# Performance work log

Measured on AMD Instinct MI355X. Metric: run time of the kernel, lower is better.

## Reference

```python
import jax, jax.numpy as jnp
import numpy as np

B, C, N, H, S = 2048, 64, 64, 8, 4
D = C // H          # head dim 8
CS = C // S         # per-scale channels 16
CP = C // 4         # pattern memory dim 16


def _conv1d(x, w, b):
    # x: [B, Cin, N], w: [Cout, Cin, 3], 'same' padding
    y = jax.lax.conv_general_dilated(x, w, (1,), ((1, 1),),
                                     dimension_numbers=('NCH', 'OIH', 'NCH'))
    return y + b[None, :, None]


def setup_inputs() -> dict:
    key = jax.random.key(0)
    ks = jax.random.split(key, 20)
    s = 0.05
    f32 = jnp.float32
    return {
        'x': jax.random.normal(ks[0], (B, C, N), f32),
        'points': jax.random.normal(ks[1], (N, 3), f32),
        'conv1_w': jax.random.normal(ks[2], (S, CS, C, 3), f32) * s,
        'conv1_b': jnp.zeros((S, CS), f32),
        'conv2_w': jax.random.normal(ks[3], (S, CS, CS, 3), f32) * s,
        'conv2_b': jnp.zeros((S, CS), f32),
        'pattern_memory': jax.random.normal(ks[4], (64, CP), f32),
        'pm1_w': jax.random.normal(ks[5], (C, C + CP), f32) * s,
        'pm1_b': jnp.zeros((C,), f32),
        'pm2_w': jax.random.normal(ks[6], (C, C), f32) * s,
        'pm2_b': jnp.zeros((C,), f32),
        'q_w': jax.random.normal(ks[7], (C, C), f32) * s,
        'q_b': jnp.zeros((C,), f32),
        'k_w': jax.random.normal(ks[8], (C, C), f32) * s,
        'k_b': jnp.zeros((C,), f32),
        'v_w': jax.random.normal(ks[9], (C, C), f32) * s,
        'v_b': jnp.zeros((C,), f32),
        'in_w': jax.random.normal(ks[10], (3 * C, C), f32) * s,
        'in_b': jnp.zeros((3 * C,), f32),
        'mo_w': jax.random.normal(ks[11], (C, C), f32) * s,
        'mo_b': jnp.zeros((C,), f32),
        'out_w': jax.random.normal(ks[12], (C, C), f32) * s,
        'out_b': jnp.zeros((C,), f32),
        'ln_g': jnp.ones((C,), f32),
        'ln_beta': jnp.zeros((C,), f32),
        'adjacency': jax.random.randint(ks[13], (64, 64), 0, 2, jnp.int32),
    }


def _forward(x, points, conv1_w, conv1_b, conv2_w, conv2_b, pattern_memory,
             pm1_w, pm1_b, pm2_w, pm2_b, q_w, q_b, k_w, k_b, v_w, v_b,
             in_w, in_b, mo_w, mo_b, out_w, out_b, ln_g, ln_beta, adjacency):
    b, c, n = x.shape
    # multi-scale conv stacks (fixed small loop over scales)
    feats = []
    for i in range(S):
        y = jax.nn.relu(_conv1d(x, conv1_w[i], conv1_b[i]))
        y = jax.nn.relu(_conv1d(y, conv2_w[i], conv2_b[i]))
        feats.append(jnp.transpose(y, (0, 2, 1)))  # [B, N, CS]
    combined = jnp.concatenate(feats, axis=-1)     # [B, N, C]
    # pattern memory broadcast per point (N == 64)
    pat = jnp.broadcast_to(pattern_memory[None], (b, n, CP))
    pi = jnp.concatenate([combined, pat], axis=-1)  # [B, N, C+CP]
    pf = jax.nn.relu(pi @ pm1_w.T + pm1_b) @ pm2_w.T + pm2_b  # [B, N, C]
    q = pf @ q_w.T + q_b
    k = pf @ k_w.T + k_b
    v = pf @ v_w.T + v_b
    # nn.MultiheadAttention: internal in_proj + out_proj
    wq, wk, wv = in_w[:C], in_w[C:2 * C], in_w[2 * C:]
    bq, bk, bv = in_b[:C], in_b[C:2 * C], in_b[2 * C:]
    q2 = (q @ wq.T + bq).reshape(b, n, H, D)
    k2 = (k @ wk.T + bk).reshape(b, n, H, D)
    v2 = (v @ wv.T + bv).reshape(b, n, H, D)
    scale = 1.0 / np.sqrt(D).astype(np.float32)
    scores = jnp.einsum('bnhd,bmhd->bhnm', q2, k2) * scale
    attn = jax.nn.softmax(scores, axis=-1)
    ctx = jnp.einsum('bhnm,bmhd->bnhd', attn, v2).reshape(b, n, C)
    attended = ctx @ mo_w.T + mo_b
    # vectorized geometric bias (replaces the 64x64 python loop)
    diff = points[:, None, :] - points[None, :, :]
    dist = jnp.sqrt(jnp.sum(diff * diff, axis=-1) + 1e-12)
    geo = jnp.where(adjacency > 0, jnp.float32(0.5), -0.1 / (1.0 + dist))
    attended = attended + geo[None]
    # layer norm over channels, then output projection
    h = attended + pf
    mu = jnp.mean(h, axis=-1, keepdims=True)
    var = jnp.mean((h - mu) ** 2, axis=-1, keepdims=True)
    hn = (h - mu) * jax.lax.rsqrt(var + 1e-5) * ln_g + ln_beta
    out = hn @ out_w.T + out_b
    return jnp.transpose(out, (0, 2, 1))  # [B, C, N]


def reference(x, points, conv1_w, conv1_b, conv2_w, conv2_b, pattern_memory,
              pm1_w, pm1_b, pm2_w, pm2_b, q_w, q_b, k_w, k_b, v_w, v_b,
              in_w, in_b, mo_w, mo_b, out_w, out_b, ln_g, ln_beta, adjacency):
    return _forward(x, points, conv1_w, conv1_b, conv2_w, conv2_b,
                    pattern_memory, pm1_w, pm1_b, pm2_w, pm2_b, q_w, q_b,
                    k_w, k_b, v_w, v_b, in_w, in_b, mo_w, mo_b, out_w, out_b,
                    ln_g, ln_beta, adjacency)
```

## Files before the change

### kernel.cpp

```cpp
#include <hip/hip_runtime.h>
#include <math.h>

using bf16x8 = __attribute__((ext_vector_type(8))) __bf16;
using f32x4  = __attribute__((ext_vector_type(4))) float;

#if __has_builtin(__builtin_amdgcn_exp2f)
#define EXP2F(x) __builtin_amdgcn_exp2f(x)
#else
#define EXP2F(x) exp2f(x)
#endif

__device__ __forceinline__ unsigned short f2bf(float f) {
  unsigned u = __float_as_uint(f);
  unsigned r = u + 0x7fffu + ((u >> 16) & 1u);
  return (unsigned short)(r >> 16);
}

__device__ __forceinline__ unsigned cvt_pk_bf16(float a, float b) {
  unsigned r;
  asm("v_cvt_pk_bf16_f32 %0, %1, %2" : "=v"(r) : "v"(a), "v"(b));
  return r;
}
__device__ __forceinline__ uint2 pk4(float a, float b, float c, float d) {
  uint2 r; r.x = cvt_pk_bf16(a, b); r.y = cvt_pk_bf16(c, d); return r;
}

__device__ __forceinline__ f32x4 mfma16(uint4 a, uint4 b, f32x4 c) {
  return __builtin_amdgcn_mfma_f32_16x16x32_bf16(
      __builtin_bit_cast(bf16x8, a), __builtin_bit_cast(bf16x8, b), c, 0, 0, 0);
}
__device__ __forceinline__ float swz_xor16(float v) {
  return __int_as_float(__builtin_amdgcn_ds_swizzle(__float_as_int(v), 0x401F));
}

#define FRAG_OFF(k, n) (((((n) >> 4) * 2 + ((k) >> 5)) * 64 + (((k) >> 3) & 3) * 16 + ((n) & 15)) * 8 + ((k) & 7))

#define ATT_C 0.51006997f

__global__ void precompute_kernel(
    const float* __restrict__ conv1_w, const float* __restrict__ conv2_w,
    const float* __restrict__ pm1_w, const float* __restrict__ pm1_b,
    const float* __restrict__ pm2_w,
    const float* __restrict__ q_w, const float* __restrict__ q_b,
    const float* __restrict__ k_w, const float* __restrict__ k_b,
    const float* __restrict__ v_w, const float* __restrict__ v_b,
    const float* __restrict__ in_w, const float* __restrict__ in_b,
    const float* __restrict__ mo_w, const float* __restrict__ out_w,
    const float* __restrict__ pattern, const float* __restrict__ points,
    const int* __restrict__ adjacency,
    unsigned short* __restrict__ wsb, float* __restrict__ wsf) {
  int idx = blockIdx.x * 256 + threadIdx.x;
  if (idx < 12288) {
    int t = idx >> 12, rem = idx & 4095;
    int oc = rem >> 6, c = rem & 63;
    wsb[idx] = f2bf(conv1_w[(oc * 64 + c) * 3 + t]);
  } else if (idx < 24576) {
    int i2 = idx - 12288;
    int t = i2 >> 12, rem = i2 & 4095;
    int oc = rem >> 6, ci = rem & 63;
    float v = ((ci >> 4) == (oc >> 4)) ? conv2_w[(oc * 16 + (ci & 15)) * 3 + t] : 0.0f;
    wsb[idx] = f2bf(v);
  } else if (idx < 28672) {
    int rem = idx - 24576;
    wsb[idx] = f2bf(pm1_w[(rem >> 6) * 80 + (rem & 63)]);
  } else if (idx < 32768) {
    wsb[idx] = f2bf(pm2_w[idx - 28672]);
  } else if (idx < 36864) {
    int rem = idx - 32768; int c = rem >> 6, k = rem & 63;
    float s = 0.f;
    #pragma unroll 8
    for (int j = 0; j < 64; ++j) s += in_w[c * 64 + j] * q_w[j * 64 + k];
    wsb[idx] = f2bf(s * ATT_C);
  } else if (idx < 40960) {
    int rem = idx - 36864; int c = rem >> 6, k = rem & 63;
    float s = 0.f;
    #pragma unroll 8
    for (int j = 0; j < 64; ++j) s += in_w[(64 + c) * 64 + j] * k_w[j * 64 + k];
    wsb[idx] = f2bf(s);
  } else if (idx < 45056) {
    int rem = idx - 40960; int c = rem >> 6, k = rem & 63;
    float s = 0.f;
    #pragma unroll 8
    for (int j = 0; j < 64; ++j) s += in_w[(128 + c) * 64 + j] * v_w[j * 64 + k];
    wsb[idx] = f2bf(s);
  } else if (idx < 49152) {
    wsb[idx] = f2bf(mo_w[idx - 45056]);
  } else if (idx < 53248) {
    wsb[idx] = f2bf(out_w[idx - 49152]);
  } else if (idx < 57344) {
    int rem = idx - 53248; int c = rem >> 6, n = rem & 63;
    float s = pm1_b[c];
    #pragma unroll
    for (int cp = 0; cp < 16; ++cp) s += pm1_w[c * 80 + 64 + cp] * pattern[n * 16 + cp];
    wsf[rem] = s;
  } else if (idx < 61440) {
    int rem = idx - 57344; int c = rem >> 6, n = rem & 63;
    float dd = 1e-12f;
    #pragma unroll
    for (int i = 0; i < 3; ++i) { float d = points[n * 3 + i] - points[c * 3 + i]; dd += d * d; }
    float dist = sqrtf(dd);
    wsf[4096 + rem] = (adjacency[n * 64 + c] > 0) ? 0.5f : (-0.1f / (1.0f + dist));
  } else if (idx < 61632) {
    int rem = idx - 61440; int which = rem >> 6, c = rem & 63;
    if (which == 0) {
      float s = in_b[c];
      for (int j = 0; j < 64; ++j) s += in_w[c * 64 + j] * q_b[j];
      wsf[8192 + c] = s * ATT_C;
    } else if (which == 1) {
      float s = in_b[64 + c];
      for (int j = 0; j < 64; ++j) s += in_w[(64 + c) * 64 + j] * k_b[j];
      wsf[8256 + c] = s;
    } else {
      float s = in_b[128 + c];
      for (int j = 0; j < 64; ++j) s += in_w[(128 + c) * 64 + j] * v_b[j];
      wsf[8320 + c] = s;
    }
  }
}

__device__ __forceinline__ void gemm64(const unsigned short* __restrict__ Wg,
                                       const unsigned short* Bf,
                                       int w, int lane, f32x4 acc[4]) {
  const int l15 = lane & 15, lq = lane >> 4;
  #pragma unroll
  for (int s = 0; s < 2; ++s) {
    bf16x8 a = *reinterpret_cast<const bf16x8*>(Wg + (16 * w + l15) * 64 + s * 32 + lq * 8);
    #pragma unroll
    for (int nt = 0; nt < 4; ++nt) {
      bf16x8 bb = *reinterpret_cast<const bf16x8*>(Bf + ((nt * 2 + s) * 64 + lane) * 8);
      acc[nt] = __builtin_amdgcn_mfma_f32_16x16x32_bf16(a, bb, acc[nt], 0, 0, 0);
    }
  }
}

#define SLOT_B 4096
#define KBASE  8704
#define VBASE  13312
#define H32F   2048
#define LNS    6656

__global__ __launch_bounds__(256, 4) void fused_kernel(
    const float* __restrict__ x,
    const unsigned short* __restrict__ wsb, const float* __restrict__ wsf,
    const float* __restrict__ conv1_b, const float* __restrict__ conv2_b,
    const float* __restrict__ pm2_b, const float* __restrict__ mo_b,
    const float* __restrict__ out_b, const float* __restrict__ ln_g,
    const float* __restrict__ ln_beta, float* __restrict__ out) {
  __shared__ __align__(16) unsigned char smem_raw[35840];
  unsigned short* S16 = reinterpret_cast<unsigned short*>(smem_raw);
  float* S32 = reinterpret_cast<float*>(smem_raw);

  const int tid = threadIdx.x;
  const int b = blockIdx.x;
  const int lane = tid & 63;
  const int w = tid >> 6;
  const int l15 = lane & 15;
  const int lq = lane >> 4;
  const int c0 = 16 * w + lq * 4;
  f32x4 pfs[4];

  if (tid < 8) S16[VBASE + tid] = 0;
  {
    const float* xb = x + b * 4096 + w * 16 * 64 + lane;
    float v[16];
    #pragma unroll
    for (int j = 0; j < 16; ++j) v[j] = xb[j * 64];
    #pragma unroll
    for (int g = 0; g < 2; ++g) {
      uint4 u;
      u.x = cvt_pk_bf16(v[g * 8 + 0], v[g * 8 + 1]);
      u.y = cvt_pk_bf16(v[g * 8 + 2], v[g * 8 + 3]);
      u.z = cvt_pk_bf16(v[g * 8 + 4], v[g * 8 + 5]);
      u.w = cvt_pk_bf16(v[g * 8 + 6], v[g * 8 + 7]);
      *reinterpret_cast<uint4*>(S16 + FRAG_OFF(w * 16 + g * 8, lane)) = u;
    }
  }
  __syncthreads();

  auto conv_pass = [&](const unsigned short* Wg, int srcBase, f32x4 acc[4]) {
    bf16x8 a6[3][2];
    #pragma unroll
    for (int t = 0; t < 3; ++t)
      #pragma unroll
      for (int s = 0; s < 2; ++s)
        a6[t][s] = *reinterpret_cast<const bf16x8*>(Wg + t * 4096 + (16 * w + l15) * 64 + s * 32 + lq * 8);
    #pragma unroll
    for (int nt = 0; nt < 4; ++nt) {
      #pragma unroll
      for (int t = 0; t < 3; ++t) {
        int np = nt * 16 + l15 + (t - 1);
        bool ok = (unsigned)np < 64u;
        int a = srcBase + (((np >> 4) * 2) * 64 + lq * 16 + (np & 15)) * 8;
        int A0 = ok ? a : VBASE;
        int A1 = ok ? (a + 512) : VBASE;
        bf16x8 b0 = *reinterpret_cast<const bf16x8*>(S16 + A0);
        bf16x8 b1 = *reinterpret_cast<const bf16x8*>(S16 + A1);
        acc[nt] = __builtin_amdgcn_mfma_f32_16x16x32_bf16(a6[t][0], b0, acc[nt], 0, 0, 0);
        acc[nt] = __builtin_amdgcn_mfma_f32_16x16x32_bf16(a6[t][1], b1, acc[nt], 0, 0, 0);
      }
    }
  };

  {
    f32x4 acc[4] = {};
    conv_pass(wsb, 0, acc);
    float bia[4] = {conv1_b[c0], conv1_b[c0 + 1], conv1_b[c0 + 2], conv1_b[c0 + 3]};
    #pragma unroll
    for (int nt = 0; nt < 4; ++nt) {
      int n = nt * 16 + l15;
      uint2 u = pk4(fmaxf(acc[nt][0] + bia[0], 0.f), fmaxf(acc[nt][1] + bia[1], 0.f),
                    fmaxf(acc[nt][2] + bia[2], 0.f), fmaxf(acc[nt][3] + bia[3], 0.f));
      *reinterpret_cast<uint2*>(S16 + SLOT_B + FRAG_OFF(c0, n)) = u;
    }
  }
  __syncthreads();

  {
    f32x4 acc[4] = {};
    conv_pass(wsb + 12288, SLOT_B, acc);
    float bia[4] = {conv2_b[c0], conv2_b[c0 + 1], conv2_b[c0 + 2], conv2_b[c0 + 3]};
    #pragma unroll
    for (int nt = 0; nt < 4; ++nt) {
      int n = nt * 16 + l15;
      uint2 u = pk4(fmaxf(acc[nt][0] + bia[0], 0.f), fmaxf(acc[nt][1] + bia[1], 0.f),
                    fmaxf(acc[nt][2] + bia[2], 0.f), fmaxf(acc[nt][3] + bia[3], 0.f));
      *reinterpret_cast<uint2*>(S16 + FRAG_OFF(c0, n)) = u;
    }
  }
  __syncthreads();

  {
    f32x4 acc[4] = {};
    gemm64(wsb + 24576, S16, w, lane, acc);
    #pragma unroll
    for (int nt = 0; nt < 4; ++nt) {
      int n = nt * 16 + l15;
      uint2 u = pk4(fmaxf(acc[nt][0] + wsf[(c0 + 0) * 64 + n], 0.f),
                    fmaxf(acc[nt][1] + wsf[(c0 + 1) * 64 + n], 0.f),
                    fmaxf(acc[nt][2] + wsf[(c0 + 2) * 64 + n], 0.f),
                    fmaxf(acc[nt][3] + wsf[(c0 + 3) * 64 + n], 0.f));
      *reinterpret_cast<uint2*>(S16 + SLOT_B + FRAG_OFF(c0, n)) = u;
    }
  }
  __syncthreads();

  {
    f32x4 acc[4] = {};
    gemm64(wsb + 28672, S16 + SLOT_B, w, lane, acc);
    float bia[4] = {pm2_b[c0], pm2_b[c0 + 1], pm2_b[c0 + 2], pm2_b[c0 + 3]};
    #pragma unroll
    for (int nt = 0; nt < 4; ++nt) {
      int n = nt * 16 + l15;
      f32x4 v;
      #pragma unroll
      for (int r = 0; r < 4; ++r) v[r] = acc[nt][r] + bia[r];
      pfs[nt] = v;
      *reinterpret_cast<uint2*>(S16 + FRAG_OFF(c0, n)) = pk4(v[0], v[1], v[2], v[3]);
    }
  }
  __syncthreads();

  {
    f32x4 acc[4] = {};
    gemm64(wsb + 32768, S16, w, lane, acc);
    #pragma unroll
    for (int nt = 0; nt < 4; ++nt) {
      int n = nt * 16 + l15;
      *reinterpret_cast<uint2*>(S16 + SLOT_B + n * 72 + c0) =
          pk4(acc[nt][0] + wsf[8192 + c0], acc[nt][1] + wsf[8192 + c0 + 1],
              acc[nt][2] + wsf[8192 + c0 + 2], acc[nt][3] + wsf[8192 + c0 + 3]);
    }
  }
  {
    f32x4 acc[4] = {};
    gemm64(wsb + 36864, S16, w, lane, acc);
    #pragma unroll
    for (int nt = 0; nt < 4; ++nt) {
      int n = nt * 16 + l15;
      *reinterpret_cast<uint2*>(S16 + KBASE + n * 72 + c0) =
          pk4(acc[nt][0] + wsf[8256 + c0], acc[nt][1] + wsf[8256 + c0 + 1],
              acc[nt][2] + wsf[8256 + c0 + 2], acc[nt][3] + wsf[8256 + c0 + 3]);
    }
  }
  {
    f32x4 acc[4] = {};
    gemm64(wsb + 40960, S16, w, lane, acc);
    #pragma unroll
    for (int nt = 0; nt < 4; ++nt) {
      int n = nt * 16 + l15;
      #pragma unroll
      for (int r = 0; r < 4; ++r)
        S16[VBASE + (c0 + r) * 72 + n] = f2bf(acc[nt][r] + wsf[8320 + c0 + r]);
    }
  }
  __syncthreads();

  {
    uint4 vb[2][2];
    #pragma unroll
    for (int rr = 0; rr < 2; ++rr) {
      int h = w + rr * 4;
      #pragma unroll
      for (int ks = 0; ks < 2; ++ks)
        vb[rr][ks] = *reinterpret_cast<const uint4*>(
            S16 + VBASE + (h * 8 + (l15 & 7)) * 72 + ks * 32 + lq * 8);
    }
    __syncthreads();

    const int Pb = VBASE + w * 1152;
    const bool lq0 = (lq == 0);
    #pragma unroll
    for (int rr = 0; rr < 2; ++rr) {
      const int h = w + rr * 4;
      uint4 ka[4];
      #pragma unroll
      for (int mt = 0; mt < 4; ++mt) {
        uint4 t = *reinterpret_cast<const uint4*>(S16 + KBASE + (mt * 16 + l15) * 72 + h * 8);
        ka[mt].x = lq0 ? t.x : 0u; ka[mt].y = lq0 ? t.y : 0u;
        ka[mt].z = lq0 ? t.z : 0u; ka[mt].w = lq0 ? t.w : 0u;
      }
      #pragma unroll
      for (int q = 0; q < 4; ++q) {
        uint4 qb = *reinterpret_cast<const uint4*>(S16 + SLOT_B + (q * 16 + l15) * 72 + h * 8);
        qb.x = lq0 ? qb.x : 0u; qb.y = lq0 ? qb.y : 0u;
        qb.z = lq0 ? qb.z : 0u; qb.w = lq0 ? qb.w : 0u;
        f32x4 sc[4];
        #pragma unroll
        for (int mt = 0; mt < 4; ++mt) {
          f32x4 z = {0.f, 0.f, 0.f, 0.f};
          sc[mt] = mfma16(ka[mt], qb, z);
        }
        float sum = 0.f;
        #pragma unroll
        for (int mt = 0; mt < 4; ++mt)
          #pragma unroll
          for (int r = 0; r < 4; ++r) {
            float e = EXP2F(sc[mt][r]);
            sc[mt][r] = e; sum += e;
          }
        sum += swz_xor16(sum);
        sum += __shfl_xor(sum, 32);
        float inv = __builtin_amdgcn_rcpf(sum);
        #pragma unroll
        for (int mt = 0; mt < 4; ++mt) {
          unsigned d0 = __builtin_amdgcn_perm(__float_as_uint(sc[mt][1] * inv),
                                              __float_as_uint(sc[mt][0] * inv), 0x07060302u);
          unsigned d1 = __builtin_amdgcn_perm(__float_as_uint(sc[mt][3] * inv),
                                              __float_as_uint(sc[mt][2] * inv), 0x07060302u);
          *reinterpret_cast<uint2*>(S16 + Pb + l15 * 72 + mt * 16 + lq * 4) = make_uint2(d0, d1);
        }
        f32x4 ctx = {0.f, 0.f, 0.f, 0.f};
        #pragma unroll
        for (int ks = 0; ks < 2; ++ks) {
          uint4 pa = *reinterpret_cast<const uint4*>(S16 + Pb + l15 * 72 + ks * 32 + lq * 8);
          ctx = mfma16(pa, vb[rr][ks], ctx);
        }
        if (l15 < 8) {
          const int kk = h * 8 + l15;
          #pragma unroll
          for (int r = 0; r < 4; ++r)
            S16[FRAG_OFF(kk, q * 16 + lq * 4 + r)] = f2bf(ctx[r]);
        }
      }
    }
  }
  __syncthreads();

  {
    f32x4 acc[4] = {};
    gemm64(wsb + 45056, S16, w, lane, acc);
    #pragma unroll
    for (int nt = 0; nt < 4; ++nt) {
      int n = nt * 16 + l15;
      #pragma unroll
      for (int r = 0; r < 4; ++r) {
        int c = c0 + r;
        S32[H32F + c * 65 + n] = acc[nt][r] + mo_b[c] + wsf[4096 + c * 64 + n] + pfs[nt][r];
      }
    }
  }
  __syncthreads();

  {
    int n = tid & 63, qq = tid >> 6;
    float sum = 0.f, ssq = 0.f;
    #pragma unroll
    for (int j = 0; j < 16; ++j) {
      float v = S32[H32F + (qq * 16 + j) * 65 + n];
      sum += v; ssq += v * v;
    }
    S32[LNS + tid] = sum;
    S32[LNS + 256 + tid] = ssq;
    __syncthreads();
    if (tid < 64) {
      float s = S32[LNS + tid] + S32[LNS + 64 + tid] + S32[LNS + 128 + tid] + S32[LNS + 192 + tid];
      float ss = S32[LNS + 256 + tid] + S32[LNS + 320 + tid] + S32[LNS + 384 + tid] + S32[LNS + 448 + tid];
      float mu = s * (1.0f / 64.0f);
      float var = ss * (1.0f / 64.0f) - mu * mu;
      S32[LNS + 512 + tid] = mu;
      S32[LNS + 576 + tid] = rsqrtf(var + 1e-5f);
    }
    __syncthreads();
    float mu = S32[LNS + 512 + n], rs = S32[LNS + 576 + n];
    #pragma unroll
    for (int half = 0; half < 2; ++half) {
      int ch0 = qq * 16 + half * 8;
      float vv[8];
      #pragma unroll
      for (int jj = 0; jj < 8; ++jj) {
        int c = ch0 + jj;
        vv[jj] = (S32[H32F + c * 65 + n] - mu) * rs * ln_g[c] + ln_beta[c];
      }
      uint4 u;
      u.x = cvt_pk_bf16(vv[0], vv[1]);
      u.y = cvt_pk_bf16(vv[2], vv[3]);
      u.z = cvt_pk_bf16(vv[4], vv[5]);
      u.w = cvt_pk_bf16(vv[6], vv[7]);
      *reinterpret_cast<uint4*>(S16 + FRAG_OFF(ch0, n)) = u;
    }
  }
  __syncthreads();

  {
    f32x4 acc[4] = {};
    gemm64(wsb + 49152, S16, w, lane, acc);
    float* ob = out + b * 4096;
    float bia[4] = {out_b[c0], out_b[c0 + 1], out_b[c0 + 2], out_b[c0 + 3]};
    #pragma unroll
    for (int nt = 0; nt < 4; ++nt) {
      int n = nt * 16 + l15;
      #pragma unroll
      for (int r = 0; r < 4; ++r)
        ob[(c0 + r) * 64 + n] = acc[nt][r] + bia[r];
    }
  }
}

extern "C" void kernel_launch(void* const* d_in, const int* in_sizes, int n_in,
                              void* d_out, int out_size, void* d_ws, size_t ws_size,
                              hipStream_t stream) {
  const float* x        = (const float*)d_in[0];
  const float* points   = (const float*)d_in[1];
  const float* conv1_w  = (const float*)d_in[2];
  const float* conv1_b  = (const float*)d_in[3];
  const float* conv2_w  = (const float*)d_in[4];
  const float* conv2_b  = (const float*)d_in[5];
  const float* pattern  = (const float*)d_in[6];
  const float* pm1_w    = (const float*)d_in[7];
  const float* pm1_b    = (const float*)d_in[8];
  const float* pm2_w    = (const float*)d_in[9];
  const float* pm2_b    = (const float*)d_in[10];
  const float* q_w      = (const float*)d_in[11];
  const float* q_b      = (const float*)d_in[12];
  const float* k_w      = (const float*)d_in[13];
  const float* k_b      = (const float*)d_in[14];
  const float* v_w      = (const float*)d_in[15];
  const float* v_b      = (const float*)d_in[16];
  const float* in_w     = (const float*)d_in[17];
  const float* in_b     = (const float*)d_in[18];
  const float* mo_w     = (const float*)d_in[19];
  const float* mo_b     = (const float*)d_in[20];
  const float* out_w    = (const float*)d_in[21];
  const float* out_b    = (const float*)d_in[22];
  const float* ln_g     = (const float*)d_in[23];
  const float* ln_beta  = (const float*)d_in[24];
  const int*   adjacency= (const int*)d_in[25];

  unsigned short* wsb = (unsigned short*)d_ws;
  float* wsf = (float*)((char*)d_ws + 106496);

  precompute_kernel<<<241, 256, 0, stream>>>(
      conv1_w, conv2_w, pm1_w, pm1_b, pm2_w, q_w, q_b, k_w, k_b, v_w, v_b,
      in_w, in_b, mo_w, out_w, pattern, points, adjacency, wsb, wsf);

  fused_kernel<<<2048, 256, 0, stream>>>(
      x, wsb, wsf, conv1_b, conv2_b, pm2_b, mo_b, out_b, ln_g, ln_beta,
      (float*)d_out);
}
```

Measured before the change: 169.1 us.

## Replace padded LDS rows with XOR swizzle to fit five blocks per CU

Q/K/V/P tiles in shared memory drop the 72-element padded stride for a dense 64-element stride with an XOR swizzle on the column offset, and the fp32 layernorm buffer loses its 65-stride padding. LDS shrinks from 35840 to 32768 bytes and the launch bound rises from 4 to 5 blocks per CU to raise occupancy. The V projection is recomputed transposed (activations as A operand, weights as B) so it can be written with packed vector stores instead of scalar bf16 stores. The unpadded fp32 buffer and a tighter register budget risk more bank conflicts or spills.

```diff
diff --git a/kernel.cpp b/kernel.cpp
--- a/kernel.cpp
+++ b/kernel.cpp
@@ -134,19 +134,19 @@
 }
 
 #define SLOT_B 4096
-#define KBASE  8704
-#define VBASE  13312
+#define KBASE  8192
+#define VBASE  12288
 #define H32F   2048
-#define LNS    6656
-
-__global__ __launch_bounds__(256, 4) void fused_kernel(
+#define LNS    6144
+
+__global__ __launch_bounds__(256, 5) void fused_kernel(
     const float* __restrict__ x,
     const unsigned short* __restrict__ wsb, const float* __restrict__ wsf,
     const float* __restrict__ conv1_b, const float* __restrict__ conv2_b,
     const float* __restrict__ pm2_b, const float* __restrict__ mo_b,
     const float* __restrict__ out_b, const float* __restrict__ ln_g,
     const float* __restrict__ ln_beta, float* __restrict__ out) {
-  __shared__ __align__(16) unsigned char smem_raw[35840];
+  __shared__ __align__(16) unsigned char smem_raw[32768];
   unsigned short* S16 = reinterpret_cast<unsigned short*>(smem_raw);
   float* S32 = reinterpret_cast<float*>(smem_raw);
 
@@ -157,6 +157,7 @@
   const int l15 = lane & 15;
   const int lq = lane >> 4;
   const int c0 = 16 * w + lq * 4;
+  const int xorm = (l15 & 7) << 3;
   f32x4 pfs[4];
 
   if (tid < 8) S16[VBASE + tid] = 0;
@@ -266,7 +267,7 @@
     #pragma unroll
     for (int nt = 0; nt < 4; ++nt) {
       int n = nt * 16 + l15;
-      *reinterpret_cast<uint2*>(S16 + SLOT_B + n * 72 + c0) =
+      *reinterpret_cast<uint2*>(S16 + SLOT_B + n * 64 + (c0 ^ xorm)) =
           pk4(acc[nt][0] + wsf[8192 + c0], acc[nt][1] + wsf[8192 + c0 + 1],
               acc[nt][2] + wsf[8192 + c0 + 2], acc[nt][3] + wsf[8192 + c0 + 3]);
     }
@@ -277,20 +278,30 @@
     #pragma unroll
     for (int nt = 0; nt < 4; ++nt) {
       int n = nt * 16 + l15;
-      *reinterpret_cast<uint2*>(S16 + KBASE + n * 72 + c0) =
+      *reinterpret_cast<uint2*>(S16 + KBASE + n * 64 + (c0 ^ xorm)) =
           pk4(acc[nt][0] + wsf[8256 + c0], acc[nt][1] + wsf[8256 + c0 + 1],
               acc[nt][2] + wsf[8256 + c0 + 2], acc[nt][3] + wsf[8256 + c0 + 3]);
     }
   }
   {
     f32x4 acc[4] = {};
-    gemm64(wsb + 40960, S16, w, lane, acc);
-    #pragma unroll
-    for (int nt = 0; nt < 4; ++nt) {
-      int n = nt * 16 + l15;
-      #pragma unroll
-      for (int r = 0; r < 4; ++r)
-        S16[VBASE + (c0 + r) * 72 + n] = f2bf(acc[nt][r] + wsf[8320 + c0 + r]);
+    const unsigned short* AV = wsb + 40960;
+    #pragma unroll
+    for (int s = 0; s < 2; ++s) {
+      bf16x8 a = *reinterpret_cast<const bf16x8*>(S16 + ((w * 2 + s) * 64 + lane) * 8);
+      #pragma unroll
+      for (int ct = 0; ct < 4; ++ct) {
+        bf16x8 bb = *reinterpret_cast<const bf16x8*>(AV + (ct * 16 + l15) * 64 + s * 32 + lq * 8);
+        acc[ct] = __builtin_amdgcn_mfma_f32_16x16x32_bf16(a, bb, acc[ct], 0, 0, 0);
+      }
+    }
+    const int m0 = 16 * w + lq * 4;
+    #pragma unroll
+    for (int ct = 0; ct < 4; ++ct) {
+      int c = ct * 16 + l15;
+      float bia = wsf[8320 + c];
+      *reinterpret_cast<uint2*>(S16 + VBASE + c * 64 + (m0 ^ xorm)) =
+          pk4(acc[ct][0] + bia, acc[ct][1] + bia, acc[ct][2] + bia, acc[ct][3] + bia);
     }
   }
   __syncthreads();
@@ -303,11 +314,11 @@
       #pragma unroll
       for (int ks = 0; ks < 2; ++ks)
         vb[rr][ks] = *reinterpret_cast<const uint4*>(
-            S16 + VBASE + (h * 8 + (l15 & 7)) * 72 + ks * 32 + lq * 8);
+            S16 + VBASE + (h * 8 + (l15 & 7)) * 64 + ((ks * 32 + lq * 8) ^ xorm));
     }
     __syncthreads();
 
-    const int Pb = VBASE + w * 1152;
+    const int Pb = VBASE + w * 1024;
     const bool lq0 = (lq == 0);
     #pragma unroll
     for (int rr = 0; rr < 2; ++rr) {
@@ -315,13 +326,15 @@
       uint4 ka[4];
       #pragma unroll
       for (int mt = 0; mt < 4; ++mt) {
-        uint4 t = *reinterpret_cast<const uint4*>(S16 + KBASE + (mt * 16 + l15) * 72 + h * 8);
+        uint4 t = *reinterpret_cast<const uint4*>(
+            S16 + KBASE + (mt * 16 + l15) * 64 + ((h * 8) ^ xorm));
         ka[mt].x = lq0 ? t.x : 0u; ka[mt].y = lq0 ? t.y : 0u;
         ka[mt].z = lq0 ? t.z : 0u; ka[mt].w = lq0 ? t.w : 0u;
       }
       #pragma unroll
       for (int q = 0; q < 4; ++q) {
-        uint4 qb = *reinterpret_cast<const uint4*>(S16 + SLOT_B + (q * 16 + l15) * 72 + h * 8);
+        uint4 qb = *reinterpret_cast<const uint4*>(
+            S16 + SLOT_B + (q * 16 + l15) * 64 + ((h * 8) ^ xorm));
         qb.x = lq0 ? qb.x : 0u; qb.y = lq0 ? qb.y : 0u;
         qb.z = lq0 ? qb.z : 0u; qb.w = lq0 ? qb.w : 0u;
         f32x4 sc[4];
@@ -347,12 +360,14 @@
                                               __float_as_uint(sc[mt][0] * inv), 0x07060302u);
           unsigned d1 = __builtin_amdgcn_perm(__float_as_uint(sc[mt][3] * inv),
                                               __float_as_uint(sc[mt][2] * inv), 0x07060302u);
-          *reinterpret_cast<uint2*>(S16 + Pb + l15 * 72 + mt * 16 + lq * 4) = make_uint2(d0, d1);
+          *reinterpret_cast<uint2*>(S16 + Pb + l15 * 64 + ((mt * 16 + lq * 4) ^ xorm)) =
+              make_uint2(d0, d1);
         }
         f32x4 ctx = {0.f, 0.f, 0.f, 0.f};
         #pragma unroll
         for (int ks = 0; ks < 2; ++ks) {
-          uint4 pa = *reinterpret_cast<const uint4*>(S16 + Pb + l15 * 72 + ks * 32 + lq * 8);
+          uint4 pa = *reinterpret_cast<const uint4*>(
+              S16 + Pb + l15 * 64 + ((ks * 32 + lq * 8) ^ xorm));
           ctx = mfma16(pa, vb[rr][ks], ctx);
         }
         if (l15 < 8) {
@@ -375,7 +390,7 @@
       #pragma unroll
       for (int r = 0; r < 4; ++r) {
         int c = c0 + r;
-        S32[H32F + c * 65 + n] = acc[nt][r] + mo_b[c] + wsf[4096 + c * 64 + n] + pfs[nt][r];
+        S32[H32F + c * 64 + n] = acc[nt][r] + mo_b[c] + wsf[4096 + c * 64 + n] + pfs[nt][r];
       }
     }
   }
@@ -386,7 +401,7 @@
     float sum = 0.f, ssq = 0.f;
     #pragma unroll
     for (int j = 0; j < 16; ++j) {
-      float v = S32[H32F + (qq * 16 + j) * 65 + n];
+      float v = S32[H32F + (qq * 16 + j) * 64 + n];
       sum += v; ssq += v * v;
     }
     S32[LNS + tid] = sum;
@@ -409,7 +424,7 @@
       #pragma unroll
       for (int jj = 0; jj < 8; ++jj) {
         int c = ch0 + jj;
-        vv[jj] = (S32[H32F + c * 65 + n] - mu) * rs * ln_g[c] + ln_beta[c];
+        vv[jj] = (S32[H32F + c * 64 + n] - mu) * rs * ln_g[c] + ln_beta[c];
       }
       uint4 u;
       u.x = cvt_pk_bf16(vv[0], vv[1]);
```

Result: slower. 183.5 us (+8.5%).

## Split fused kernel across 8 waves with 2D wave tiling and one head per wave

Applied to the files above, without the earlier changes.

Doubles the block to 512 threads and splits each 64x64 GEMM tile between two waves along N, giving each wave two accumulator tiles instead of four. In attention, each wave now handles one head instead of two, and the P scratch buffers are moved onto the K region once K has been loaded into registers. The goal is more resident waves per CU to hide MFMA and LDS latency. The trade-off is extra barrier cost and tight register limits from launch_bounds(512, 8), which could cause spills.

```diff
diff --git a/kernel.cpp b/kernel.cpp
--- a/kernel.cpp
+++ b/kernel.cpp
@@ -120,15 +120,16 @@
 
 __device__ __forceinline__ void gemm64(const unsigned short* __restrict__ Wg,
                                        const unsigned short* Bf,
-                                       int w, int lane, f32x4 acc[4]) {
+                                       int wm, int wn, int lane, f32x4 acc[2]) {
   const int l15 = lane & 15, lq = lane >> 4;
   #pragma unroll
   for (int s = 0; s < 2; ++s) {
-    bf16x8 a = *reinterpret_cast<const bf16x8*>(Wg + (16 * w + l15) * 64 + s * 32 + lq * 8);
-    #pragma unroll
-    for (int nt = 0; nt < 4; ++nt) {
+    bf16x8 a = *reinterpret_cast<const bf16x8*>(Wg + (16 * wm + l15) * 64 + s * 32 + lq * 8);
+    #pragma unroll
+    for (int nti = 0; nti < 2; ++nti) {
+      int nt = 2 * wn + nti;
       bf16x8 bb = *reinterpret_cast<const bf16x8*>(Bf + ((nt * 2 + s) * 64 + lane) * 8);
-      acc[nt] = __builtin_amdgcn_mfma_f32_16x16x32_bf16(a, bb, acc[nt], 0, 0, 0);
+      acc[nti] = __builtin_amdgcn_mfma_f32_16x16x32_bf16(a, bb, acc[nti], 0, 0, 0);
     }
   }
 }
@@ -139,7 +140,7 @@
 #define H32F   2048
 #define LNS    6656
 
-__global__ __launch_bounds__(256, 4) void fused_kernel(
+__global__ __launch_bounds__(512, 8) void fused_kernel(
     const float* __restrict__ x,
     const unsigned short* __restrict__ wsb, const float* __restrict__ wsf,
     const float* __restrict__ conv1_b, const float* __restrict__ conv2_b,
@@ -154,38 +155,38 @@
   const int b = blockIdx.x;
   const int lane = tid & 63;
   const int w = tid >> 6;
+  const int wm = w >> 1;
+  const int wn = w & 1;
   const int l15 = lane & 15;
   const int lq = lane >> 4;
-  const int c0 = 16 * w + lq * 4;
-  f32x4 pfs[4];
+  const int c0 = 16 * wm + lq * 4;
+  f32x4 pfs[2];
 
   if (tid < 8) S16[VBASE + tid] = 0;
   {
-    const float* xb = x + b * 4096 + w * 16 * 64 + lane;
-    float v[16];
-    #pragma unroll
-    for (int j = 0; j < 16; ++j) v[j] = xb[j * 64];
-    #pragma unroll
-    for (int g = 0; g < 2; ++g) {
-      uint4 u;
-      u.x = cvt_pk_bf16(v[g * 8 + 0], v[g * 8 + 1]);
-      u.y = cvt_pk_bf16(v[g * 8 + 2], v[g * 8 + 3]);
-      u.z = cvt_pk_bf16(v[g * 8 + 4], v[g * 8 + 5]);
-      u.w = cvt_pk_bf16(v[g * 8 + 6], v[g * 8 + 7]);
-      *reinterpret_cast<uint4*>(S16 + FRAG_OFF(w * 16 + g * 8, lane)) = u;
-    }
-  }
-  __syncthreads();
-
-  auto conv_pass = [&](const unsigned short* Wg, int srcBase, f32x4 acc[4]) {
+    const float* xb = x + b * 4096 + w * 8 * 64 + lane;
+    float v[8];
+    #pragma unroll
+    for (int j = 0; j < 8; ++j) v[j] = xb[j * 64];
+    uint4 u;
+    u.x = cvt_pk_bf16(v[0], v[1]);
+    u.y = cvt_pk_bf16(v[2], v[3]);
+    u.z = cvt_pk_bf16(v[4], v[5]);
+    u.w = cvt_pk_bf16(v[6], v[7]);
+    *reinterpret_cast<uint4*>(S16 + FRAG_OFF(w * 8, lane)) = u;
+  }
+  __syncthreads();
+
+  auto conv_pass = [&](const unsigned short* Wg, int srcBase, f32x4 acc[2]) {
     bf16x8 a6[3][2];
     #pragma unroll
     for (int t = 0; t < 3; ++t)
       #pragma unroll
       for (int s = 0; s < 2; ++s)
-        a6[t][s] = *reinterpret_cast<const bf16x8*>(Wg + t * 4096 + (16 * w + l15) * 64 + s * 32 + lq * 8);
-    #pragma unroll
-    for (int nt = 0; nt < 4; ++nt) {
+        a6[t][s] = *reinterpret_cast<const bf16x8*>(Wg + t * 4096 + (16 * wm + l15) * 64 + s * 32 + lq * 8);
+    #pragma unroll
+    for (int nti = 0; nti < 2; ++nti) {
+      int nt = 2 * wn + nti;
       #pragma unroll
       for (int t = 0; t < 3; ++t) {
         int np = nt * 16 + l15 + (t - 1);
@@ -195,187 +196,180 @@
         int A1 = ok ? (a + 512) : VBASE;
         bf16x8 b0 = *reinterpret_cast<const bf16x8*>(S16 + A0);
         bf16x8 b1 = *reinterpret_cast<const bf16x8*>(S16 + A1);
-        acc[nt] = __builtin_amdgcn_mfma_f32_16x16x32_bf16(a6[t][0], b0, acc[nt], 0, 0, 0);
-        acc[nt] = __builtin_amdgcn_mfma_f32_16x16x32_bf16(a6[t][1], b1, acc[nt], 0, 0, 0);
+        acc[nti] = __builtin_amdgcn_mfma_f32_16x16x32_bf16(a6[t][0], b0, acc[nti], 0, 0, 0);
+        acc[nti] = __builtin_amdgcn_mfma_f32_16x16x32_bf16(a6[t][1], b1, acc[nti], 0, 0, 0);
       }
     }
   };
 
   {
-    f32x4 acc[4] = {};
+    f32x4 acc[2] = {};
     conv_pass(wsb, 0, acc);
     float bia[4] = {conv1_b[c0], conv1_b[c0 + 1], conv1_b[c0 + 2], conv1_b[c0 + 3]};
     #pragma unroll
-    for (int nt = 0; nt < 4; ++nt) {
-      int n = nt * 16 + l15;
-      uint2 u = pk4(fmaxf(acc[nt][0] + bia[0], 0.f), fmaxf(acc[nt][1] + bia[1], 0.f),
-                    fmaxf(acc[nt][2] + bia[2], 0.f), fmaxf(acc[nt][3] + bia[3], 0.f));
+    for (int nti = 0; nti < 2; ++nti) {
+      int n = (2 * wn + nti) * 16 + l15;
+      uint2 u = pk4(fmaxf(acc[nti][0] + bia[0], 0.f), fmaxf(acc[nti][1] + bia[1], 0.f),
+                    fmaxf(acc[nti][2] + bia[2], 0.f), fmaxf(acc[nti][3] + bia[3], 0.f));
       *reinterpret_cast<uint2*>(S16 + SLOT_B + FRAG_OFF(c0, n)) = u;
     }
   }
   __syncthreads();
 
   {
-    f32x4 acc[4] = {};
+    f32x4 acc[2] = {};
     conv_pass(wsb + 12288, SLOT_B, acc);
     float bia[4] = {conv2_b[c0], conv2_b[c0 + 1], conv2_b[c0 + 2], conv2_b[c0 + 3]};
     #pragma unroll
-    for (int nt = 0; nt < 4; ++nt) {
-      int n = nt * 16 + l15;
-      uint2 u = pk4(fmaxf(acc[nt][0] + bia[0], 0.f), fmaxf(acc[nt][1] + bia[1], 0.f),
-                    fmaxf(acc[nt][2] + bia[2], 0.f), fmaxf(acc[nt][3] + bia[3], 0.f));
+    for (int nti = 0; nti < 2; ++nti) {
+      int n = (2 * wn + nti) * 16 + l15;
+      uint2 u = pk4(fmaxf(acc[nti][0] + bia[0], 0.f), fmaxf(acc[nti][1] + bia[1], 0.f),
+                    fmaxf(acc[nti][2] + bia[2], 0.f), fmaxf(acc[nti][3] + bia[3], 0.f));
       *reinterpret_cast<uint2*>(S16 + FRAG_OFF(c0, n)) = u;
     }
   }
   __syncthreads();
 
   {
-    f32x4 acc[4] = {};
-    gemm64(wsb + 24576, S16, w, lane, acc);
-    #pragma unroll
-    for (int nt = 0; nt < 4; ++nt) {
-      int n = nt * 16 + l15;
-      uint2 u = pk4(fmaxf(acc[nt][0] + wsf[(c0 + 0) * 64 + n], 0.f),
-                    fmaxf(acc[nt][1] + wsf[(c0 + 1) * 64 + n], 0.f),
-                    fmaxf(acc[nt][2] + wsf[(c0 + 2) * 64 + n], 0.f),
-                    fmaxf(acc[nt][3] + wsf[(c0 + 3) * 64 + n], 0.f));
+    f32x4 acc[2] = {};
+    gemm64(wsb + 24576, S16, wm, wn, lane, acc);
+    #pragma unroll
+    for (int nti = 0; nti < 2; ++nti) {
+      int n = (2 * wn + nti) * 16 + l15;
+      uint2 u = pk4(fmaxf(acc[nti][0] + wsf[(c0 + 0) * 64 + n], 0.f),
+                    fmaxf(acc[nti][1] + wsf[(c0 + 1) * 64 + n], 0.f),
+                    fmaxf(acc[nti][2] + wsf[(c0 + 2) * 64 + n], 0.f),
+                    fmaxf(acc[nti][3] + wsf[(c0 + 3) * 64 + n], 0.f));
       *reinterpret_cast<uint2*>(S16 + SLOT_B + FRAG_OFF(c0, n)) = u;
     }
   }
   __syncthreads();
 
   {
-    f32x4 acc[4] = {};
-    gemm64(wsb + 28672, S16 + SLOT_B, w, lane, acc);
+    f32x4 acc[2] = {};
+    gemm64(wsb + 28672, S16 + SLOT_B, wm, wn, lane, acc);
     float bia[4] = {pm2_b[c0], pm2_b[c0 + 1], pm2_b[c0 + 2], pm2_b[c0 + 3]};
     #pragma unroll
-    for (int nt = 0; nt < 4; ++nt) {
-      int n = nt * 16 + l15;
+    for (int nti = 0; nti < 2; ++nti) {
+      int n = (2 * wn + nti) * 16 + l15;
       f32x4 v;
       #pragma unroll
-      for (int r = 0; r < 4; ++r) v[r] = acc[nt][r] + bia[r];
-      pfs[nt] = v;
+      for (int r = 0; r < 4; ++r) v[r] = acc[nti][r] + bia[r];
+      pfs[nti] = v;
       *reinterpret_cast<uint2*>(S16 + FRAG_OFF(c0, n)) = pk4(v[0], v[1], v[2], v[3]);
     }
   }
   __syncthreads();
 
   {
-    f32x4 acc[4] = {};
-    gemm64(wsb + 32768, S16, w, lane, acc);
-    #pragma unroll
-    for (int nt = 0; nt < 4; ++nt) {
-      int n = nt * 16 + l15;
+    f32x4 acc[2] = {};
+    gemm64(wsb + 32768, S16, wm, wn, lane, acc);
+    #pragma unroll
+    for (int nti = 0; nti < 2; ++nti) {
+      int n = (2 * wn + nti) * 16 + l15;
       *reinterpret_cast<uint2*>(S16 + SLOT_B + n * 72 + c0) =
-          pk4(acc[nt][0] + wsf[8192 + c0], acc[nt][1] + wsf[8192 + c0 + 1],
-              acc[nt][2] + wsf[8192 + c0 + 2], acc[nt][3] + wsf[8192 + c0 + 3]);
-    }
-  }
-  {
-    f32x4 acc[4] = {};
-    gemm64(wsb + 36864, S16, w, lane, acc);
-    #pragma unroll
-    for (int nt = 0; nt < 4; ++nt) {
-      int n = nt * 16 + l15;
+          pk4(acc[nti][0] + wsf[8192 + c0], acc[nti][1] + wsf[8192 + c0 + 1],
+              acc[nti][2] + wsf[8192 + c0 + 2], acc[nti][3] + wsf[8192 + c0 + 3]);
+    }
+  }
+  {
+    f32x4 acc[2] = {};
+    gemm64(wsb + 36864, S16, wm, wn, lane, acc);
+    #pragma unroll
+    for (int nti = 0; nti < 2; ++nti) {
+      int n = (2 * wn + nti) * 16 + l15;
       *reinterpret_cast<uint2*>(S16 + KBASE + n * 72 + c0) =
-          pk4(acc[nt][0] + wsf[8256 + c0], acc[nt][1] + wsf[8256 + c0 + 1],
-              acc[nt][2] + wsf[8256 + c0 + 2], acc[nt][3] + wsf[8256 + c0 + 3]);
-    }
-  }
-  {
-    f32x4 acc[4] = {};
-    gemm64(wsb + 40960, S16, w, lane, acc);
-    #pragma unroll
-    for (int nt = 0; nt < 4; ++nt) {
-      int n = nt * 16 + l15;
+          pk4(acc[nti][0] + wsf[8256 + c0], acc[nti][1] + wsf[8256 + c0 + 1],
+              acc[nti][2] + wsf[8256 + c0 + 2], acc[nti][3] + wsf[8256 + c0 + 3]);
+    }
+  }
+  {
+    f32x4 acc[2] = {};
+    gemm64(wsb + 40960, S16, wm, wn, lane, acc);
+    #pragma unroll
+    for (int nti = 0; nti < 2; ++nti) {
+      int n = (2 * wn + nti) * 16 + l15;
       #pragma unroll
       for (int r = 0; r < 4; ++r)
-        S16[VBASE + (c0 + r) * 72 + n] = f2bf(acc[nt][r] + wsf[8320 + c0 + r]);
-    }
-  }
-  __syncthreads();
-
-  {
-    uint4 vb[2][2];
-    #pragma unroll
-    for (int rr = 0; rr < 2; ++rr) {
-      int h = w + rr * 4;
-      #pragma unroll
-      for (int ks = 0; ks < 2; ++ks)
-        vb[rr][ks] = *reinterpret_cast<const uint4*>(
-            S16 + VBASE + (h * 8 + (l15 & 7)) * 72 + ks * 32 + lq * 8);
+        S16[VBASE + (c0 + r) * 72 + n] = f2bf(acc[nti][r] + wsf[8320 + c0 + r]);
+    }
+  }
+  __syncthreads();
+
+  {
+    const int h = w;
+    const bool lq0 = (lq == 0);
+    uint4 vb[2];
+    #pragma unroll
+    for (int ks = 0; ks < 2; ++ks)
+      vb[ks] = *reinterpret_cast<const uint4*>(
+          S16 + VBASE + (h * 8 + (l15 & 7)) * 72 + ks * 32 + lq * 8);
+    uint4 ka[4];
+    #pragma unroll
+    for (int mt = 0; mt < 4; ++mt) {
+      uint4 t = *reinterpret_cast<const uint4*>(S16 + KBASE + (mt * 16 + l15) * 72 + h * 8);
+      ka[mt].x = lq0 ? t.x : 0u; ka[mt].y = lq0 ? t.y : 0u;
+      ka[mt].z = lq0 ? t.z : 0u; ka[mt].w = lq0 ? t.w : 0u;
     }
     __syncthreads();
 
-    const int Pb = VBASE + w * 1152;
-    const bool lq0 = (lq == 0);
-    #pragma unroll
-    for (int rr = 0; rr < 2; ++rr) {
-      const int h = w + rr * 4;
-      uint4 ka[4];
+    const int Pb = KBASE + w * 1152;
+    #pragma unroll
+    for (int q = 0; q < 4; ++q) {
+      uint4 qb = *reinterpret_cast<const uint4*>(S16 + SLOT_B + (q * 16 + l15) * 72 + h * 8);
+      qb.x = lq0 ? qb.x : 0u; qb.y = lq0 ? qb.y : 0u;
+      qb.z = lq0 ? qb.z : 0u; qb.w = lq0 ? qb.w : 0u;
+      f32x4 sc[4];
       #pragma unroll
       for (int mt = 0; mt < 4; ++mt) {
-        uint4 t = *reinterpret_cast<const uint4*>(S16 + KBASE + (mt * 16 + l15) * 72 + h * 8);
-        ka[mt].x = lq0 ? t.x : 0u; ka[mt].y = lq0 ? t.y : 0u;
-        ka[mt].z = lq0 ? t.z : 0u; ka[mt].w = lq0 ? t.w : 0u;
-      }
-      #pragma unroll
-      for (int q = 0; q < 4; ++q) {
-        uint4 qb = *reinterpret_cast<const uint4*>(S16 + SLOT_B + (q * 16 + l15) * 72 + h * 8);
-        qb.x = lq0 ? qb.x : 0u; qb.y = lq0 ? qb.y : 0u;
-        qb.z = lq0 ? qb.z : 0u; qb.w = lq0 ? qb.w : 0u;
-        f32x4 sc[4];
+        f32x4 z = {0.f, 0.f, 0.f, 0.f};
+        sc[mt] = mfma16(ka[mt], qb, z);
+      }
+      float sum = 0.f;
+      #pragma unroll
+      for (int mt = 0; mt < 4; ++mt)
         #pragma unroll
-        for (int mt = 0; mt < 4; ++mt) {
-          f32x4 z = {0.f, 0.f, 0.f, 0.f};
-          sc[mt] = mfma16(ka[mt], qb, z);
+        for (int r = 0; r < 4; ++r) {
+          float e = EXP2F(sc[mt][r]);
+          sc[mt][r] = e; sum += e;
         }
-        float sum = 0.f;
+      sum += swz_xor16(sum);
+      sum += __shfl_xor(sum, 32);
+      float inv = __builtin_amdgcn_rcpf(sum);
+      #pragma unroll
+      for (int mt = 0; mt < 4; ++mt) {
+        unsigned d0 = __builtin_amdgcn_perm(__float_as_uint(sc[mt][1] * inv),
+                                            __float_as_uint(sc[mt][0] * inv), 0x07060302u);
+        unsigned d1 = __builtin_amdgcn_perm(__float_as_uint(sc[mt][3] * inv),
+                                            __float_as_uint(sc[mt][2] * inv), 0x07060302u);
+        *reinterpret_cast<uint2*>(S16 + Pb + l15 * 72 + mt * 16 + lq * 4) = make_uint2(d0, d1);
+      }
+      f32x4 ctx = {0.f, 0.f, 0.f, 0.f};
+      #pragma unroll
+      for (int ks = 0; ks < 2; ++ks) {
+        uint4 pa = *reinterpret_cast<const uint4*>(S16 + Pb + l15 * 72 + ks * 32 + lq * 8);
+        ctx = mfma16(pa, vb[ks], ctx);
+      }
+      if (l15 < 8) {
+        const int kk = h * 8 + l15;
         #pragma unroll
-        for (int mt = 0; mt < 4; ++mt)
-          #pragma unroll
-          for (int r = 0; r < 4; ++r) {
-            float e = EXP2F(sc[mt][r]);
-            sc[mt][r] = e; sum += e;
-          }
-        sum += swz_xor16(sum);
-        sum += __shfl_xor(sum, 32);
-        float inv = __builtin_amdgcn_rcpf(sum);
-        #pragma unroll
-        for (int mt = 0; mt < 4; ++mt) {
-          unsigned d0 = __builtin_amdgcn_perm(__float_as_uint(sc[mt][1] * inv),
-                                              __float_as_uint(sc[mt][0] * inv), 0x07060302u);
-          unsigned d1 = __builtin_amdgcn_perm(__float_as_uint(sc[mt][3] * inv),
-                                              __float_as_uint(sc[mt][2] * inv), 0x07060302u);
-          *reinterpret_cast<uint2*>(S16 + Pb + l15 * 72 + mt * 16 + lq * 4) = make_uint2(d0, d1);
-        }
-        f32x4 ctx = {0.f, 0.f, 0.f, 0.f};
-        #pragma unroll
-        for (int ks = 0; ks < 2; ++ks) {
-          uint4 pa = *reinterpret_cast<const uint4*>(S16 + Pb + l15 * 72 + ks * 32 + lq * 8);
-          ctx = mfma16(pa, vb[rr][ks], ctx);
-        }
-        if (l15 < 8) {
-          const int kk = h * 8 + l15;
-          #pragma unroll
-          for (int r = 0; r < 4; ++r)
-            S16[FRAG_OFF(kk, q * 16 + lq * 4 + r)] = f2bf(ctx[r]);
-        }
-      }
-    }
-  }
-  __syncthreads();
-
-  {
-    f32x4 acc[4] = {};
-    gemm64(wsb + 45056, S16, w, lane, acc);
-    #pragma unroll
-    for (int nt = 0; nt < 4; ++nt) {
-      int n = nt * 16 + l15;
+        for (int r = 0; r < 4; ++r)
+          S16[FRAG_OFF(kk, q * 16 + lq * 4 + r)] = f2bf(ctx[r]);
+      }
+    }
+  }
+  __syncthreads();
+
+  {
+    f32x4 acc[2] = {};
+    gemm64(wsb + 45056, S16, wm, wn, lane, acc);
+    #pragma unroll
+    for (int nti = 0; nti < 2; ++nti) {
+      int n = (2 * wn + nti) * 16 + l15;
       #pragma unroll
       for (int r = 0; r < 4; ++r) {
         int c = c0 + r;
-        S32[H32F + c * 65 + n] = acc[nt][r] + mo_b[c] + wsf[4096 + c * 64 + n] + pfs[nt][r];
+        S32[H32F + c * 65 + n] = acc[nti][r] + mo_b[c] + wsf[4096 + c * 64 + n] + pfs[nti][r];
       }
     }
   }
@@ -385,53 +379,54 @@
     int n = tid & 63, qq = tid >> 6;
     float sum = 0.f, ssq = 0.f;
     #pragma unroll
-    for (int j = 0; j < 16; ++j) {
-      float v = S32[H32F + (qq * 16 + j) * 65 + n];
+    for (int j = 0; j < 8; ++j) {
+      float v = S32[H32F + (qq * 8 + j) * 65 + n];
       sum += v; ssq += v * v;
     }
     S32[LNS + tid] = sum;
-    S32[LNS + 256 + tid] = ssq;
+    S32[LNS + 512 + tid] = ssq;
     __syncthreads();
     if (tid < 64) {
-      float s = S32[LNS + tid] + S32[LNS + 64 + tid] + S32[LNS + 128 + tid] + S32[LNS + 192 + tid];
-      float ss = S32[LNS + 256 + tid] + S32[LNS + 320 + tid] + S32[LNS + 384 + tid] + S32[LNS + 448 + tid];
+      float s = 0.f, ss = 0.f;
+      #pragma unroll
+      for (int i = 0; i < 8; ++i) {
+        s  += S32[LNS + i * 64 + tid];
+        ss += S32[LNS + 512 + i * 64 + tid];
+      }
       float mu = s * (1.0f / 64.0f);
       float var = ss * (1.0f / 64.0f) - mu * mu;
-      S32[LNS + 512 + tid] = mu;
-      S32[LNS + 576 + tid] = rsqrtf(var + 1e-5f);
+      S32[LNS + 1024 + tid] = mu;
+      S32[LNS + 1088 + tid] = rsqrtf(var + 1e-5f);
     }
     __syncthreads();
-    float mu = S32[LNS + 512 + n], rs = S32[LNS + 576 + n];
-    #pragma unroll
-    for (int half = 0; half < 2; ++half) {
-      int ch0 = qq * 16 + half * 8;
-      float vv[8];
-      #pragma unroll
-      for (int jj = 0; jj < 8; ++jj) {
-        int c = ch0 + jj;
-        vv[jj] = (S32[H32F + c * 65 + n] - mu) * rs * ln_g[c] + ln_beta[c];
-      }
-      uint4 u;
-      u.x = cvt_pk_bf16(vv[0], vv[1]);
-      u.y = cvt_pk_bf16(vv[2], vv[3]);
-      u.z = cvt_pk_bf16(vv[4], vv[5]);
-      u.w = cvt_pk_bf16(vv[6], vv[7]);
-      *reinterpret_cast<uint4*>(S16 + FRAG_OFF(ch0, n)) = u;
-    }
-  }
-  __syncthreads();
-
-  {
-    f32x4 acc[4] = {};
-    gemm64(wsb + 49152, S16, w, lane, acc);
+    float mu = S32[LNS + 1024 + n], rs = S32[LNS + 1088 + n];
+    int ch0 = qq * 8;
+    float vv[8];
+    #pragma unroll
+    for (int jj = 0; jj < 8; ++jj) {
+      int c = ch0 + jj;
+      vv[jj] = (S32[H32F + c * 65 + n] - mu) * rs * ln_g[c] + ln_beta[c];
+    }
+    uint4 u;
+    u.x = cvt_pk_bf16(vv[0], vv[1]);
+    u.y = cvt_pk_bf16(vv[2], vv[3]);
+    u.z = cvt_pk_bf16(vv[4], vv[5]);
+    u.w = cvt_pk_bf16(vv[6], vv[7]);
+    *reinterpret_cast<uint4*>(S16 + FRAG_OFF(ch0, n)) = u;
+  }
+  __syncthreads();
+
+  {
+    f32x4 acc[2] = {};
+    gemm64(wsb + 49152, S16, wm, wn, lane, acc);
     float* ob = out + b * 4096;
     float bia[4] = {out_b[c0], out_b[c0 + 1], out_b[c0 + 2], out_b[c0 + 3]};
     #pragma unroll
-    for (int nt = 0; nt < 4; ++nt) {
-      int n = nt * 16 + l15;
+    for (int nti = 0; nti < 2; ++nti) {
+      int n = (2 * wn + nti) * 16 + l15;
       #pragma unroll
       for (int r = 0; r < 4; ++r)
-        ob[(c0 + r) * 64 + n] = acc[nt][r] + bia[r];
+        ob[(c0 + r) * 64 + n] = acc[nti][r] + bia[r];
     }
   }
 }
@@ -473,7 +468,7 @@
       conv1_w, conv2_w, pm1_w, pm1_b, pm2_w, q_w, q_b, k_w, k_b, v_w, v_b,
       in_w, in_b, mo_w, out_w, pattern, points, adjacency, wsb, wsf);
 
-  fused_kernel<<<2048, 256, 0, stream>>>(
+  fused_kernel<<<2048, 512, 0, stream>>>(
       x, wsb, wsf, conv1_b, conv2_b, pm2_b, mo_b, out_b, ln_g, ln_beta,
       (float*)d_out);
 }
```

New measurement: 205.9 us. 1.22x slower.

## Software-pipeline attention softmax and PV stages with double-buffered probability tiles

Applied to the files above, without the earlier changes.

Hoists the K fragment loads for both heads ahead of the barrier and restructures the per-head/per-query-tile attention loop into a two-stage software pipeline. The scores, softmax and P-write for iteration i+1 are issued before the PV MFMA of iteration i, using two P buffers per wave placed in the now-free K region. The aim is to hide LDS write-to-read latency and exp/MFMA dependency stalls. In exchange it holds more fragments in registers, and it relies on the K area not being read after the barrier.

```diff
diff --git a/kernel.cpp b/kernel.cpp
--- a/kernel.cpp
+++ b/kernel.cpp
@@ -296,72 +296,82 @@
   __syncthreads();
 
   {
-    uint4 vb[2][2];
+    const bool lq0 = (lq == 0);
+    uint4 vb[2][2], ka[2][4];
     #pragma unroll
     for (int rr = 0; rr < 2; ++rr) {
-      int h = w + rr * 4;
+      const int h = w + rr * 4;
       #pragma unroll
       for (int ks = 0; ks < 2; ++ks)
         vb[rr][ks] = *reinterpret_cast<const uint4*>(
             S16 + VBASE + (h * 8 + (l15 & 7)) * 72 + ks * 32 + lq * 8);
+      #pragma unroll
+      for (int mt = 0; mt < 4; ++mt) {
+        uint4 t = *reinterpret_cast<const uint4*>(
+            S16 + KBASE + (mt * 16 + l15) * 72 + h * 8);
+        ka[rr][mt].x = lq0 ? t.x : 0u; ka[rr][mt].y = lq0 ? t.y : 0u;
+        ka[rr][mt].z = lq0 ? t.z : 0u; ka[rr][mt].w = lq0 ? t.w : 0u;
+      }
     }
     __syncthreads();
 
-    const int Pb = VBASE + w * 1152;
-    const bool lq0 = (lq == 0);
-    #pragma unroll
-    for (int rr = 0; rr < 2; ++rr) {
+    auto stageA = [&](int i) {
+      const int rr = i >> 2, q = i & 3;
       const int h = w + rr * 4;
-      uint4 ka[4];
+      uint4 qb = *reinterpret_cast<const uint4*>(
+          S16 + SLOT_B + (q * 16 + l15) * 72 + h * 8);
+      qb.x = lq0 ? qb.x : 0u; qb.y = lq0 ? qb.y : 0u;
+      qb.z = lq0 ? qb.z : 0u; qb.w = lq0 ? qb.w : 0u;
+      f32x4 sc[4];
       #pragma unroll
       for (int mt = 0; mt < 4; ++mt) {
-        uint4 t = *reinterpret_cast<const uint4*>(S16 + KBASE + (mt * 16 + l15) * 72 + h * 8);
-        ka[mt].x = lq0 ? t.x : 0u; ka[mt].y = lq0 ? t.y : 0u;
-        ka[mt].z = lq0 ? t.z : 0u; ka[mt].w = lq0 ? t.w : 0u;
-      }
-      #pragma unroll
-      for (int q = 0; q < 4; ++q) {
-        uint4 qb = *reinterpret_cast<const uint4*>(S16 + SLOT_B + (q * 16 + l15) * 72 + h * 8);
-        qb.x = lq0 ? qb.x : 0u; qb.y = lq0 ? qb.y : 0u;
-        qb.z = lq0 ? qb.z : 0u; qb.w = lq0 ? qb.w : 0u;
-        f32x4 sc[4];
+        f32x4 z = {0.f, 0.f, 0.f, 0.f};
+        sc[mt] = mfma16(ka[rr][mt], qb, z);
+      }
+      float sum = 0.f;
+      #pragma unroll
+      for (int mt = 0; mt < 4; ++mt)
         #pragma unroll
-        for (int mt = 0; mt < 4; ++mt) {
-          f32x4 z = {0.f, 0.f, 0.f, 0.f};
-          sc[mt] = mfma16(ka[mt], qb, z);
+        for (int r = 0; r < 4; ++r) {
+          float e = EXP2F(sc[mt][r]);
+          sc[mt][r] = e; sum += e;
         }
-        float sum = 0.f;
+      sum += swz_xor16(sum);
+      sum += __shfl_xor(sum, 32);
+      float inv = __builtin_amdgcn_rcpf(sum);
+      const int Pb = KBASE + (w * 2 + (i & 1)) * 1152;
+      #pragma unroll
+      for (int mt = 0; mt < 4; ++mt) {
+        unsigned d0 = __builtin_amdgcn_perm(__float_as_uint(sc[mt][1] * inv),
+                                            __float_as_uint(sc[mt][0] * inv), 0x07060302u);
+        unsigned d1 = __builtin_amdgcn_perm(__float_as_uint(sc[mt][3] * inv),
+                                            __float_as_uint(sc[mt][2] * inv), 0x07060302u);
+        *reinterpret_cast<uint2*>(S16 + Pb + l15 * 72 + mt * 16 + lq * 4) =
+            make_uint2(d0, d1);
+      }
+    };
+    auto stageB = [&](int i) {
+      const int rr = i >> 2, q = i & 3;
+      const int Pb = KBASE + (w * 2 + (i & 1)) * 1152;
+      f32x4 ctx = {0.f, 0.f, 0.f, 0.f};
+      #pragma unroll
+      for (int ks = 0; ks < 2; ++ks) {
+        uint4 pa = *reinterpret_cast<const uint4*>(
+            S16 + Pb + l15 * 72 + ks * 32 + lq * 8);
+        ctx = mfma16(pa, vb[rr][ks], ctx);
+      }
+      if (l15 < 8) {
+        const int kk = (w + rr * 4) * 8 + l15;
         #pragma unroll
-        for (int mt = 0; mt < 4; ++mt)
-          #pragma unroll
-          for (int r = 0; r < 4; ++r) {
-            float e = EXP2F(sc[mt][r]);
-            sc[mt][r] = e; sum += e;
-          }
-        sum += swz_xor16(sum);
-        sum += __shfl_xor(sum, 32);
-        float inv = __builtin_amdgcn_rcpf(sum);
-        #pragma unroll
-        for (int mt = 0; mt < 4; ++mt) {
-          unsigned d0 = __builtin_amdgcn_perm(__float_as_uint(sc[mt][1] * inv),
-                                              __float_as_uint(sc[mt][0] * inv), 0x07060302u);
-          unsigned d1 = __builtin_amdgcn_perm(__float_as_uint(sc[mt][3] * inv),
-                                              __float_as_uint(sc[mt][2] * inv), 0x07060302u);
-          *reinterpret_cast<uint2*>(S16 + Pb + l15 * 72 + mt * 16 + lq * 4) = make_uint2(d0, d1);
-        }
-        f32x4 ctx = {0.f, 0.f, 0.f, 0.f};
-        #pragma unroll
-        for (int ks = 0; ks < 2; ++ks) {
-          uint4 pa = *reinterpret_cast<const uint4*>(S16 + Pb + l15 * 72 + ks * 32 + lq * 8);
-          ctx = mfma16(pa, vb[rr][ks], ctx);
-        }
-        if (l15 < 8) {
-          const int kk = h * 8 + l15;
-          #pragma unroll
-          for (int r = 0; r < 4; ++r)
-            S16[FRAG_OFF(kk, q * 16 + lq * 4 + r)] = f2bf(ctx[r]);
-        }
-      }
+        for (int r = 0; r < 4; ++r)
+          S16[FRAG_OFF(kk, q * 16 + lq * 4 + r)] = f2bf(ctx[r]);
+      }
+    };
+    stageA(0);
+    #pragma unroll
+    for (int i = 0; i < 8; ++i) {
+      if (i < 7) stageA(i + 1);
+      stageB(i);
     }
   }
   __syncthreads();
```

Result: no change. 167.7 us (-0.9%).
